# Kernel optimization log

Measured on AMD Instinct MI355X. Metric: run time of the kernel, lower is better.

Reference implementation:

```python
import jax, jax.numpy as jnp
import numpy as np
from jax import lax

NB = 8          # num_blocks
THRESH = 0.01   # sparsity_threshold


def _clinear(z, wr, wi, bias):
    # complex linear y = z @ W^T + b with W = wr + i*wi, z complex
    # (c+id)(a+ib) = (ca - db) + i(cb + da)  -- same math as the torch
    # Karatsuba decomposition (k1-k3, k1+k2).
    zr, zi = z.real, z.imag
    yr = jnp.einsum('...i,oi->...o', zr, wr) - jnp.einsum('...i,oi->...o', zi, wi)
    yi = jnp.einsum('...i,oi->...o', zr, wi) + jnp.einsum('...i,oi->...o', zi, wr)
    y = lax.complex(yr, yi)
    return y + lax.complex(bias[:, 0], bias[:, 1])


def _softshrink(v, t):
    return jnp.where(v > t, v - t, jnp.where(v < -t, v + t, jnp.zeros_like(v)))


def setup_inputs() -> dict:
    key = jax.random.key(0)
    ks = jax.random.split(key, 7)
    B, H, W, D = 4, 128, 128, 768
    bs = D // NB          # block_size = 96
    hid = bs              # hidden_size_factor = 1.0
    scale = np.sqrt(0.5).astype(np.float32)
    kaiming = 1.0 / np.sqrt(bs)
    x = jax.random.normal(ks[0], (B, H, W, D), dtype=jnp.float32)
    # ComplexLinear weights: nn.Linear init then scaled by sqrt(0.5)
    w1r = jax.random.uniform(ks[1], (hid, bs), jnp.float32, -kaiming, kaiming) * scale
    w1i = jax.random.uniform(ks[2], (hid, bs), jnp.float32, -kaiming, kaiming) * scale
    b1 = jax.random.normal(ks[3], (hid, 2), dtype=jnp.float32) * 0.02
    kaiming2 = 1.0 / np.sqrt(hid)
    w2r = jax.random.uniform(ks[4], (bs, hid), jnp.float32, -kaiming2, kaiming2) * scale
    w2i = jax.random.uniform(ks[5], (bs, hid), jnp.float32, -kaiming2, kaiming2) * scale
    b2 = jax.random.normal(ks[6], (bs, 2), dtype=jnp.float32) * 0.02
    return {"x": x, "w1r": w1r, "w1i": w1i, "b1": b1,
            "w2r": w2r, "w2i": w2i, "b2": b2}


def reference(x, w1r, w1i, b1, w2r, w2i, b2):
    B, H, W, D = x.shape
    bs = D // NB
    bias = x  # direct_skip=True -> identity skip
    # ortho-normalized real FFT over spatial dims (1,2)
    xf = jnp.fft.rfftn(x, s=(H, W), axes=(1, 2), norm='ortho')  # [B,H,Fw,D] c64
    Fw = xf.shape[2]
    xb = xf.reshape(B, H, Fw, NB, bs)
    h = _clinear(xb, w1r, w1i, b1)
    h = lax.complex(jax.nn.relu(h.real), jax.nn.relu(h.imag))  # ComplexReLU
    y = _clinear(h, w2r, w2i, b2)
    y = y.reshape(B, H, Fw, D)
    # componentwise softshrink (by_magnitude=False)
    y = lax.complex(_softshrink(y.real, THRESH), _softshrink(y.imag, THRESH))
    out = jnp.fft.irfftn(y, s=(H, W), axes=(1, 2), norm='ortho')
    return out + bias
```

## Files before the change

### kernel.cpp

```cpp
#include <hip/hip_runtime.h>
#include <hip/hip_bf16.h>
#include <cstdio>

#define TPB 256
#define B_ 4
#define H_ 128
#define W_ 128
#define D_ 768
#define FW 65
#define BH_ 512
#define THRESH_ 0.01f
#define NEG_TWO_PI_OVER_128 (-0.04908738521234052f)

typedef short bf16x8 __attribute__((ext_vector_type(8)));
typedef float f32x4 __attribute__((ext_vector_type(4)));


__device__ __forceinline__ unsigned pk(float lo, float hi) {
  __hip_bfloat162 h2 = __float22bfloat162_rn(make_float2(lo, hi));
  return *(unsigned*)&h2;
}
__device__ __forceinline__ float2 upk(unsigned u) {
  return __bfloat1622float2(*(__hip_bfloat162*)&u);
}
__device__ __forceinline__ int drev(int k) {
  return ((k & 3) << 5) | (((k >> 2) & 3) << 3) | (((k >> 4) & 3) << 1) | ((k >> 6) & 1);
}

template <bool FWD>
__device__ __forceinline__ void bfly4(float* re, float* im, int i0, int i1, int i2, int i3,
                                      float c1, float s1, float c2, float s2, float c3, float s3) {
  const float x0r = re[i0], x0i = im[i0], x1r = re[i1], x1i = im[i1];
  const float x2r = re[i2], x2i = im[i2], x3r = re[i3], x3i = im[i3];
  const float v0r = x0r + x2r, v0i = x0i + x2i, v2r = x0r - x2r, v2i = x0i - x2i;
  const float v1r = x1r + x3r, v1i = x1i + x3i, v3r = x1r - x3r, v3i = x1i - x3i;
  float u1r, u1i, u3r, u3i;
  if (FWD) { u1r = v2r + v3i; u1i = v2i - v3r; u3r = v2r - v3i; u3i = v2i + v3r; }
  else     { u1r = v2r - v3i; u1i = v2i + v3r; u3r = v2r + v3i; u3i = v2i - v3r; }
  const float u2r = v0r - v1r, u2i = v0i - v1i;
  re[i0] = v0r + v1r; im[i0] = v0i + v1i;
  re[i1] = u1r * c1 - u1i * s1; im[i1] = u1r * s1 + u1i * c1;
  re[i2] = u2r * c2 - u2i * s2; im[i2] = u2r * s2 + u2i * c2;
  re[i3] = u3r * c3 - u3i * s3; im[i3] = u3r * s3 + u3i * c3;
}

template <bool FWD>
__device__ __forceinline__ void run_stage(float* re, float* im, int t,
                                          int npmask, int npbits, int span, int twm,
                                          const float* twr, const float* twi) {
#pragma unroll
  for (int it = 0; it < 4; ++it) {
    const int gid = it * TPB + t;
    const int cc = gid & 31, g = gid >> 5;
    const int np = g & npmask, blk = g >> npbits;
    const int base = blk * (span << 2) + np;
    const int i0 = base * 32 + cc, i1 = (base + span) * 32 + cc;
    const int i2 = (base + 2 * span) * 32 + cc, i3 = (base + 3 * span) * 32 + cc;
    const int tb = np * twm;
    float c1 = twr[tb], s1 = twi[tb];
    float c2 = twr[2 * tb], s2 = twi[2 * tb];
    float c3 = twr[3 * tb], s3 = twi[3 * tb];
    if (!FWD) { s1 = -s1; s2 = -s2; s3 = -s3; }
    bfly4<FWD>(re, im, i0, i1, i2, i3, c1, s1, c2, s2, c3, s3);
  }
  __syncthreads();
}

__device__ __forceinline__ void run_stage_dit(float* re, float* im, int t,
                                              int npmask, int npbits, int span, int twm,
                                              const float* twr, const float* twi) {
#pragma unroll
  for (int it = 0; it < 4; ++it) {
    const int gid = it * TPB + t;
    const int cc = gid & 31, g = gid >> 5;
    const int np = g & npmask, blk = g >> npbits;
    const int base = blk * (span << 2) + np;
    const int i0 = base * 32 + cc, i1 = (base + span) * 32 + cc;
    const int i2 = (base + 2 * span) * 32 + cc, i3 = (base + 3 * span) * 32 + cc;
    const int tb = np * twm;
    const float c1 = twr[tb], s1 = twi[tb];
    const float c2 = twr[2 * tb], s2 = twi[2 * tb];
    const float c3 = twr[3 * tb], s3 = twi[3 * tb];
    const float t0r = re[i0], t0i = im[i0];
    const float y1r = re[i1], y1i = im[i1], y2r = re[i2], y2i = im[i2], y3r = re[i3], y3i = im[i3];
    const float t1r = y1r * c1 + y1i * s1, t1i = y1i * c1 - y1r * s1;
    const float t2r = y2r * c2 + y2i * s2, t2i = y2i * c2 - y2r * s2;
    const float t3r = y3r * c3 + y3i * s3, t3i = y3i * c3 - y3r * s3;
    const float w0r = t0r + t2r, w0i = t0i + t2i, w2r = t0r - t2r, w2i = t0i - t2i;
    const float w1r = t1r + t3r, w1i = t1i + t3i, w3r = t1r - t3r, w3i = t1i - t3i;
    re[i0] = w0r + w1r; im[i0] = w0i + w1i;
    re[i1] = w2r - w3i; im[i1] = w2i + w3r;
    re[i2] = w0r - w1r; im[i2] = w0i - w1i;
    re[i3] = w2r + w3i; im[i3] = w2i - w3r;
  }
  __syncthreads();
}

__device__ __forceinline__ void run_r2(float* re, float* im, int t) {
#pragma unroll
  for (int it = 0; it < 8; ++it) {
    const int pid = it * TPB + t;
    const int cc = pid & 31, p = pid >> 5;
    const int i0 = (2 * p) * 32 + cc, i1 = i0 + 32;
    const float ar = re[i0], ai = im[i0], br = re[i1], bi = im[i1];
    re[i0] = ar + br; im[i0] = ai + bi;
    re[i1] = ar - br; im[i1] = ai - bi;
  }
  __syncthreads();
}

#define TW_INIT() do { if (t < 128) { float s_, c_; \
    __sincosf(NEG_TWO_PI_OVER_128 * (float)t, &s_, &c_); twr[t] = c_; twi[t] = s_; } } while (0)

__global__ __launch_bounds__(TPB) void k_wpack(const float* __restrict__ w1r,
                                               const float* __restrict__ w1i,
                                               const float* __restrict__ w2r,
                                               const float* __restrict__ w2i,
                                               unsigned short* __restrict__ wp) {
  const int tid = blockIdx.x * TPB + threadIdx.x;
  if (tid >= 2 * 36864) return;
  const int L = tid / 36864, rem = tid % 36864;
  const int n = rem / 192, k = rem % 192;
  const int c = k >> 1, s = k & 1, o = n >> 1, t = n & 1;
  const float* wr = L ? w2r : w1r;
  const float* wi = L ? w2i : w1i;
  const float val = (s == 0) ? (t == 0 ? wr[o * 96 + c] : wi[o * 96 + c])
                             : (t == 0 ? -wi[o * 96 + c] : wr[o * 96 + c]);
  __hip_bfloat16 h = __float2bfloat16(val);
  const int idx = ((n * 6 + (k >> 5)) * 4 + ((k >> 3) & 3)) * 8 + (k & 7);
  wp[L * 36864 + idx] = *(unsigned short*)&h;
}

__global__ __launch_bounds__(TPB) void k_fwd_w(const float* __restrict__ x,
                                               unsigned* __restrict__ fq) {
  __shared__ float re[4096], im[4096], twr[128], twi[128];
  const int t = threadIdx.x;
  const int bh = blockIdx.x;
  const int d0 = blockIdx.y << 6;
  TW_INIT();
  const float2* xp = (const float2*)(x + (size_t)bh * 98304 + d0);
#pragma unroll
  for (int it = 0; it < 16; ++it) {
    const int w = (it << 3) + (t >> 5), c = t & 31;
    const float2 v = xp[w * 384 + c];
    re[w * 32 + c] = v.x; im[w * 32 + c] = v.y;
  }
  __syncthreads();
  run_stage<true>(re, im, t, 31, 5, 32, 1, twr, twi);
  run_stage<true>(re, im, t, 7, 3, 8, 4, twr, twi);
  run_stage<true>(re, im, t, 1, 1, 2, 16, twr, twi);
  run_r2(re, im, t);
#pragma unroll
  for (int it = 0; it < 9; ++it) {
    const int idx = it * TPB + t;
    if (idx < FW * 32) {
      const int q = idx >> 5, c = idx & 31;
      const int sq = drev(q), sm = drev((128 - q) & 127);
      const float a = re[sq * 32 + c], b = im[sq * 32 + c];
      const float cr = re[sm * 32 + c], dr = -im[sm * 32 + c];
      const float hsc = 0.00390625f;
      const float xer = (a + cr) * hsc, xei = (b + dr) * hsc;
      const float xor_ = (b - dr) * hsc, xoi = (cr - a) * hsc;
      *(uint2*)(fq + (size_t)(bh * FW + q) * 768 + d0 + 2 * c) =
          make_uint2(pk(xer, xei), pk(xor_, xoi));
    }
  }
}

__global__ __launch_bounds__(TPB) void k_fwd_h(unsigned* __restrict__ fq) {
  __shared__ float re[4096], im[4096], twr[128], twi[128];
  const int t = threadIdx.x;
  const int b = blockIdx.x, fw = blockIdx.y, d0 = blockIdx.z << 5;
  TW_INIT();
  unsigned* fp = fq + (size_t)(b * 128 * FW + fw) * 768 + d0;
#pragma unroll
  for (int it = 0; it < 16; ++it) {
    const int h = (it << 3) + (t >> 5), c = t & 31;
    const float2 v = upk(fp[(size_t)h * (FW * 768) + c]);
    re[h * 32 + c] = v.x; im[h * 32 + c] = v.y;
  }
  __syncthreads();
  run_stage<true>(re, im, t, 31, 5, 32, 1, twr, twi);
  run_stage<true>(re, im, t, 7, 3, 8, 4, twr, twi);
  run_stage<true>(re, im, t, 1, 1, 2, 16, twr, twi);
  run_r2(re, im, t);
#pragma unroll
  for (int it = 0; it < 16; ++it) {
    const int h = (it << 3) + (t >> 5), c = t & 31;
    fp[(size_t)h * (FW * 768) + c] = pk(re[h * 32 + c], im[h * 32 + c]);
  }
}

__global__ __launch_bounds__(TPB, 2) void k_mlp_mfma(unsigned* __restrict__ fq,
    const bf16x8* __restrict__ wpb,
    const float* __restrict__ b1, const float* __restrict__ b2) {
  __shared__ __align__(16) char lds[49152];
  const int t  = threadIdx.x;
  const int wv = t >> 6;
  const int l  = t & 63;
  const int c16 = l & 15, g = l >> 4, low3 = l & 7;
  const int n0 = wv * 48;
  const int P0 = blockIdx.x << 7;

  const uint4* src = (const uint4*)(fq + (size_t)P0 * 96);
#pragma unroll
  for (int it = 0; it < 12; ++it) {
    const int q = it * TPB + t;
    const int row = q / 24, f = q % 24;
    *(uint4*)(lds + row * 384 + ((f * 16) ^ ((row & 7) << 4))) = src[q];
  }
  __syncthreads();

  f32x4 acc[8][3];
  float bs0 = b1[n0 + c16], bs1 = b1[n0 + 16 + c16], bs2 = b1[n0 + 32 + c16];

#pragma unroll
  for (int mt = 0; mt < 8; ++mt)
#pragma unroll
    for (int np = 0; np < 3; ++np) acc[mt][np] = (f32x4)0.f;
  for (int kk = 0; kk < 6; ++kk) {
    bf16x8 a[8];
#pragma unroll
    for (int mt = 0; mt < 8; ++mt) {
      const int row = (mt << 4) + c16;
      a[mt] = *(const bf16x8*)(lds + row * 384 + ((kk * 64 + g * 16) ^ (low3 << 4)));
    }
    bf16x8 bfr[3];
#pragma unroll
    for (int np = 0; np < 3; ++np) bfr[np] = wpb[((n0 + np * 16 + c16) * 6 + kk) * 4 + g];
#pragma unroll
    for (int mt = 0; mt < 8; ++mt)
#pragma unroll
      for (int np = 0; np < 3; ++np)
        acc[mt][np] = __builtin_amdgcn_mfma_f32_16x16x32_bf16(a[mt], bfr[np], acc[mt][np], 0, 0, 0);
  }
  __syncthreads();
#pragma unroll
  for (int mt = 0; mt < 8; ++mt)
#pragma unroll
    for (int np = 0; np < 3; ++np) {
      const int col = n0 + np * 16 + c16;
      const float bb = np == 0 ? bs0 : (np == 1 ? bs1 : bs2);
#pragma unroll
      for (int r = 0; r < 4; ++r) {
        const int row = (mt << 4) + (g << 2) + r;
        const float vv = fmaxf(acc[mt][np][r] + bb, 0.f);
        __hip_bfloat16 hb = __float2bfloat16(vv);
        *(unsigned short*)(lds + row * 384 + ((2 * col) ^ ((row & 7) << 4))) = *(unsigned short*)&hb;
      }
    }
  __syncthreads();

  bs0 = b2[n0 + c16]; bs1 = b2[n0 + 16 + c16]; bs2 = b2[n0 + 32 + c16];
#pragma unroll
  for (int mt = 0; mt < 8; ++mt)
#pragma unroll
    for (int np = 0; np < 3; ++np) acc[mt][np] = (f32x4)0.f;
  const bf16x8* wpb2 = wpb + 4608;
  for (int kk = 0; kk < 6; ++kk) {
    bf16x8 a[8];
#pragma unroll
    for (int mt = 0; mt < 8; ++mt) {
      const int row = (mt << 4) + c16;
      a[mt] = *(const bf16x8*)(lds + row * 384 + ((kk * 64 + g * 16) ^ (low3 << 4)));
    }
    bf16x8 bfr[3];
#pragma unroll
    for (int np = 0; np < 3; ++np) bfr[np] = wpb2[((n0 + np * 16 + c16) * 6 + kk) * 4 + g];
#pragma unroll
    for (int mt = 0; mt < 8; ++mt)
#pragma unroll
      for (int np = 0; np < 3; ++np)
        acc[mt][np] = __builtin_amdgcn_mfma_f32_16x16x32_bf16(a[mt], bfr[np], acc[mt][np], 0, 0, 0);
  }
  unsigned short* fq16 = (unsigned short*)fq;
#pragma unroll
  for (int mt = 0; mt < 8; ++mt)
#pragma unroll
    for (int np = 0; np < 3; ++np) {
      const int col = n0 + np * 16 + c16;
      const float bb = np == 0 ? bs0 : (np == 1 ? bs1 : bs2);
#pragma unroll
      for (int r = 0; r < 4; ++r) {
        const int row = (mt << 4) + (g << 2) + r;
        float vv = acc[mt][np][r] + bb;
        vv = (vv > THRESH_) ? (vv - THRESH_) : ((vv < -THRESH_) ? (vv + THRESH_) : 0.f);
        __hip_bfloat16 hb = __float2bfloat16(vv);
        fq16[(size_t)(P0 + row) * 192 + col] = *(unsigned short*)&hb;
      }
    }
}

__global__ __launch_bounds__(TPB) void k_inv_h(unsigned* __restrict__ fq) {
  __shared__ float re[4096], im[4096], twr[128], twi[128];
  const int t = threadIdx.x;
  const int b = blockIdx.x, fw = blockIdx.y, d0 = blockIdx.z << 5;
  TW_INIT();
  unsigned* fp = fq + (size_t)(b * 128 * FW + fw) * 768 + d0;
#pragma unroll
  for (int it = 0; it < 16; ++it) {
    const int h = (it << 3) + (t >> 5), c = t & 31;
    const float2 v = upk(fp[(size_t)h * (FW * 768) + c]);
    re[h * 32 + c] = v.x; im[h * 32 + c] = v.y;
  }
  __syncthreads();
  run_r2(re, im, t);
  run_stage_dit(re, im, t, 1, 1, 2, 16, twr, twi);
  run_stage_dit(re, im, t, 7, 3, 8, 4, twr, twi);
  run_stage_dit(re, im, t, 31, 5, 32, 1, twr, twi);
#pragma unroll
  for (int it = 0; it < 16; ++it) {
    const int h = (it << 3) + (t >> 5), c = t & 31;
    fp[(size_t)h * (FW * 768) + c] = pk(re[h * 32 + c], im[h * 32 + c]);
  }
}

__global__ __launch_bounds__(TPB) void k_inv_w(const unsigned* __restrict__ fq,
                                               const float* __restrict__ x,
                                               float* __restrict__ out) {
  __shared__ float re[4096], im[4096], twr[128], twi[128];
  const int t = threadIdx.x;
  const int bh = blockIdx.x;
  const int d0 = blockIdx.y << 6;
  TW_INIT();
#pragma unroll
  for (int it = 0; it < 9; ++it) {
    const int idx = it * TPB + t;
    if (idx < FW * 32) {
      const int q = idx >> 5, c = idx & 31;
      const uint2 vv = *(const uint2*)(fq + (size_t)(bh * FW + q) * 768 + d0 + 2 * c);
      const float2 e = upk(vv.x), o = upk(vv.y);
      re[q * 32 + c] = e.x - o.y; im[q * 32 + c] = e.y + o.x;
      if (q >= 1 && q <= 63) {
        re[(128 - q) * 32 + c] = e.x + o.y;
        im[(128 - q) * 32 + c] = o.x - e.y;
      }
    }
  }
  __syncthreads();
  run_stage<false>(re, im, t, 31, 5, 32, 1, twr, twi);
  run_stage<false>(re, im, t, 7, 3, 8, 4, twr, twi);
  run_stage<false>(re, im, t, 1, 1, 2, 16, twr, twi);
  run_r2(re, im, t);
  const float sc = 0.0078125f;
#pragma unroll
  for (int it = 0; it < 16; ++it) {
    const int w = (it << 3) + (t >> 5), c = t & 31;
    const int s = drev(w);
    const float yr = re[s * 32 + c] * sc, yi = im[s * 32 + c] * sc;
    const size_t fi = (size_t)bh * 49152 + w * 384 + (d0 >> 1) + c;
    const float2 xv = ((const float2*)x)[fi];
    ((float2*)out)[fi] = make_float2(yr + xv.x, yi + xv.y);
  }
}

extern "C" void kernel_launch(void* const* d_in, const int* in_sizes, int n_in,
                              void* d_out, int out_size, void* d_ws, size_t ws_size,
                              hipStream_t stream) {
  const float* x   = (const float*)d_in[0];
  const float* w1r = (const float*)d_in[1];
  const float* w1i = (const float*)d_in[2];
  const float* b1  = (const float*)d_in[3];
  const float* w2r = (const float*)d_in[4];
  const float* w2i = (const float*)d_in[5];
  const float* b2  = (const float*)d_in[6];
  unsigned* fq = (unsigned*)d_ws;
  float* out = (float*)d_out;

  const size_t need = (size_t)BH_ * FW * 768 * 4;
  if (ws_size < need) {
    fprintf(stderr, "kernel_launch: ws too small (%zu < %zu)\n", ws_size, need);
    return;
  }

  unsigned short* wp = (unsigned short*)d_out;

  k_wpack<<<dim3(288), TPB, 0, stream>>>(w1r, w1i, w2r, w2i, wp);
  k_fwd_w<<<dim3(BH_, 12), TPB, 0, stream>>>(x, fq);
  k_fwd_h<<<dim3(B_, FW, 24), TPB, 0, stream>>>(fq);
  k_mlp_mfma<<<dim3(2080), TPB, 0, stream>>>(fq, (const bf16x8*)wp, b1, b2);
  k_inv_h<<<dim3(B_, FW, 24), TPB, 0, stream>>>(fq);
  k_inv_w<<<dim3(BH_, 12), TPB, 0, stream>>>(fq, x, out);
}
```

Measured before the change: 354.7 us.

## Fuse H-axis FFT, complex MLP and inverse H-axis FFT into one kernel

Merges the forward column FFT, both complex-linear MFMA layers and the inverse column FFT into a single 512-thread kernel. Each block holds one 128x96 channel block for one (b, fw) in LDS as fp32 with a swizzled layout. The MLP reads its operands directly from the FFT result and writes the hidden activations back to LDS. This removes two global round trips of the bf16 spectrum and two kernel launches. In exchange, each block uses about 99KB of LDS, which allows only one block per CU. The grid also shrinks to 2080 blocks of 512 threads, which may reduce latency hiding.

```diff
diff --git a/kernel.cpp b/kernel.cpp
--- a/kernel.cpp
+++ b/kernel.cpp
@@ -66,17 +66,63 @@
   __syncthreads();
 }
 
-__device__ __forceinline__ void run_stage_dit(float* re, float* im, int t,
-                                              int npmask, int npbits, int span, int twm,
-                                              const float* twr, const float* twi) {
-#pragma unroll
-  for (int it = 0; it < 4; ++it) {
-    const int gid = it * TPB + t;
-    const int cc = gid & 31, g = gid >> 5;
+__device__ __forceinline__ void run_r2(float* re, float* im, int t) {
+#pragma unroll
+  for (int it = 0; it < 8; ++it) {
+    const int pid = it * TPB + t;
+    const int cc = pid & 31, p = pid >> 5;
+    const int i0 = (2 * p) * 32 + cc, i1 = i0 + 32;
+    const float ar = re[i0], ai = im[i0], br = re[i1], bi = im[i1];
+    re[i0] = ar + br; im[i0] = ai + bi;
+    re[i1] = ar - br; im[i1] = ai - bi;
+  }
+  __syncthreads();
+}
+
+#define TW_INIT() do { if (t < 128) { float s_, c_; \
+    __sincosf(NEG_TWO_PI_OVER_128 * (float)t, &s_, &c_); twr[t] = c_; twi[t] = s_; } } while (0)
+
+__device__ __forceinline__ int midx(int s, int c) { return s * 96 + (c ^ ((s & 7) << 2)); }
+
+template <bool FWD>
+__device__ __forceinline__ void stage512(float* re, float* im, int t,
+                                         int npmask, int npbits, int span, int twm,
+                                         const float* twr, const float* twi) {
+#pragma unroll
+  for (int it = 0; it < 6; ++it) {
+    const int gid = it * 512 + t;
+    const int c5 = gid & 31;
+    const int rest = gid >> 5;
+    const int g = rest & 31, cblk = rest >> 5;
+    const int col = cblk * 32 + c5;
     const int np = g & npmask, blk = g >> npbits;
     const int base = blk * (span << 2) + np;
-    const int i0 = base * 32 + cc, i1 = (base + span) * 32 + cc;
-    const int i2 = (base + 2 * span) * 32 + cc, i3 = (base + 3 * span) * 32 + cc;
+    const int i0 = midx(base, col), i1 = midx(base + span, col);
+    const int i2 = midx(base + 2 * span, col), i3 = midx(base + 3 * span, col);
+    const int tb = np * twm;
+    float c1 = twr[tb], s1 = twi[tb];
+    float c2 = twr[2 * tb], s2 = twi[2 * tb];
+    float c3 = twr[3 * tb], s3 = twi[3 * tb];
+    if (!FWD) { s1 = -s1; s2 = -s2; s3 = -s3; }
+    bfly4<FWD>(re, im, i0, i1, i2, i3, c1, s1, c2, s2, c3, s3);
+  }
+  __syncthreads();
+}
+
+__device__ __forceinline__ void dit512(float* re, float* im, int t,
+                                       int npmask, int npbits, int span, int twm,
+                                       const float* twr, const float* twi) {
+#pragma unroll
+  for (int it = 0; it < 6; ++it) {
+    const int gid = it * 512 + t;
+    const int c5 = gid & 31;
+    const int rest = gid >> 5;
+    const int g = rest & 31, cblk = rest >> 5;
+    const int col = cblk * 32 + c5;
+    const int np = g & npmask, blk = g >> npbits;
+    const int base = blk * (span << 2) + np;
+    const int i0 = midx(base, col), i1 = midx(base + span, col);
+    const int i2 = midx(base + 2 * span, col), i3 = midx(base + 3 * span, col);
     const int tb = np * twm;
     const float c1 = twr[tb], s1 = twi[tb];
     const float c2 = twr[2 * tb], s2 = twi[2 * tb];
@@ -96,21 +142,21 @@
   __syncthreads();
 }
 
-__device__ __forceinline__ void run_r2(float* re, float* im, int t) {
-#pragma unroll
-  for (int it = 0; it < 8; ++it) {
-    const int pid = it * TPB + t;
-    const int cc = pid & 31, p = pid >> 5;
-    const int i0 = (2 * p) * 32 + cc, i1 = i0 + 32;
+__device__ __forceinline__ void r2_512(float* re, float* im, int t) {
+#pragma unroll
+  for (int it = 0; it < 12; ++it) {
+    const int gid = it * 512 + t;
+    const int c5 = gid & 31;
+    const int rest = gid >> 5;
+    const int p = rest & 63, cblk = rest >> 6;
+    const int col = cblk * 32 + c5;
+    const int i0 = midx(2 * p, col), i1 = midx(2 * p + 1, col);
     const float ar = re[i0], ai = im[i0], br = re[i1], bi = im[i1];
     re[i0] = ar + br; im[i0] = ai + bi;
     re[i1] = ar - br; im[i1] = ai - bi;
   }
   __syncthreads();
 }
-
-#define TW_INIT() do { if (t < 128) { float s_, c_; \
-    __sincosf(NEG_TWO_PI_OVER_128 * (float)t, &s_, &c_); twr[t] = c_; twi[t] = s_; } } while (0)
 
 __global__ __launch_bounds__(TPB) void k_wpack(const float* __restrict__ w1r,
                                                const float* __restrict__ w1i,
@@ -167,151 +213,154 @@
   }
 }
 
-__global__ __launch_bounds__(TPB) void k_fwd_h(unsigned* __restrict__ fq) {
-  __shared__ float re[4096], im[4096], twr[128], twi[128];
-  const int t = threadIdx.x;
-  const int b = blockIdx.x, fw = blockIdx.y, d0 = blockIdx.z << 5;
-  TW_INIT();
-  unsigned* fp = fq + (size_t)(b * 128 * FW + fw) * 768 + d0;
-#pragma unroll
-  for (int it = 0; it < 16; ++it) {
-    const int h = (it << 3) + (t >> 5), c = t & 31;
-    const float2 v = upk(fp[(size_t)h * (FW * 768) + c]);
-    re[h * 32 + c] = v.x; im[h * 32 + c] = v.y;
-  }
-  __syncthreads();
-  run_stage<true>(re, im, t, 31, 5, 32, 1, twr, twi);
-  run_stage<true>(re, im, t, 7, 3, 8, 4, twr, twi);
-  run_stage<true>(re, im, t, 1, 1, 2, 16, twr, twi);
-  run_r2(re, im, t);
-#pragma unroll
-  for (int it = 0; it < 16; ++it) {
-    const int h = (it << 3) + (t >> 5), c = t & 31;
-    fp[(size_t)h * (FW * 768) + c] = pk(re[h * 32 + c], im[h * 32 + c]);
-  }
-}
-
-__global__ __launch_bounds__(TPB, 2) void k_mlp_mfma(unsigned* __restrict__ fq,
+__global__ __launch_bounds__(512, 1) void k_mid(unsigned* __restrict__ fq,
     const bf16x8* __restrict__ wpb,
     const float* __restrict__ b1, const float* __restrict__ b2) {
-  __shared__ __align__(16) char lds[49152];
-  const int t  = threadIdx.x;
-  const int wv = t >> 6;
-  const int l  = t & 63;
-  const int c16 = l & 15, g = l >> 4, low3 = l & 7;
-  const int n0 = wv * 48;
-  const int P0 = blockIdx.x << 7;
-
-  const uint4* src = (const uint4*)(fq + (size_t)P0 * 96);
+  extern __shared__ float sm[];
+  float* re  = sm;
+  float* im  = sm + 12288;
+  float* twr = sm + 24576;
+  float* twi = sm + 24704;
+  const int t = threadIdx.x;
+  const int blk = blockIdx.x, fw = blockIdx.y, b = blockIdx.z;
+  TW_INIT();
+  unsigned* fp = fq + ((size_t)(b * 128) * FW + fw) * 768 + blk * 96;
+
 #pragma unroll
   for (int it = 0; it < 12; ++it) {
-    const int q = it * TPB + t;
-    const int row = q / 24, f = q % 24;
-    *(uint4*)(lds + row * 384 + ((f * 16) ^ ((row & 7) << 4))) = src[q];
-  }
-  __syncthreads();
-
-  f32x4 acc[8][3];
-  float bs0 = b1[n0 + c16], bs1 = b1[n0 + 16 + c16], bs2 = b1[n0 + 32 + c16];
-
-#pragma unroll
-  for (int mt = 0; mt < 8; ++mt)
+    const int gid = it * 512 + t;
+    const int uc = gid % 48, h = gid / 48;
+    const uint2 v = *(const uint2*)(fp + (size_t)h * (FW * 768) + 2 * uc);
+    const float2 e0 = upk(v.x), e1 = upk(v.y);
+    const int idx = midx(h, 2 * uc);
+    *(float2*)(re + idx) = make_float2(e0.x, e1.x);
+    *(float2*)(im + idx) = make_float2(e0.y, e1.y);
+  }
+  __syncthreads();
+
+  stage512<true>(re, im, t, 31, 5, 32, 1, twr, twi);
+  stage512<true>(re, im, t, 7, 3, 8, 4, twr, twi);
+  stage512<true>(re, im, t, 1, 1, 2, 16, twr, twi);
+  r2_512(re, im, t);
+
+  const int wv = t >> 6, l = t & 63;
+  const int c16 = l & 15, g4 = l >> 4;
+  const int wr = wv >> 2, wc = wv & 3;
+  const int n0 = wc * 48, row0 = wr * 64;
+
+  float bA[3], bB[3];
+#pragma unroll
+  for (int np = 0; np < 3; ++np) {
+    bA[np] = b1[n0 + np * 16 + c16];
+    bB[np] = b2[n0 + np * 16 + c16];
+  }
+
+  f32x4 acc[4][3];
+#pragma unroll
+  for (int mt = 0; mt < 4; ++mt)
 #pragma unroll
     for (int np = 0; np < 3; ++np) acc[mt][np] = (f32x4)0.f;
+
   for (int kk = 0; kk < 6; ++kk) {
-    bf16x8 a[8];
-#pragma unroll
-    for (int mt = 0; mt < 8; ++mt) {
-      const int row = (mt << 4) + c16;
-      a[mt] = *(const bf16x8*)(lds + row * 384 + ((kk * 64 + g * 16) ^ (low3 << 4)));
+    bf16x8 a[4];
+#pragma unroll
+    for (int mt = 0; mt < 4; ++mt) {
+      const int row = row0 + mt * 16 + c16;
+      const int idx = midx(row, kk * 16 + g4 * 4);
+      const f32x4 r4 = *(const f32x4*)(re + idx);
+      const f32x4 i4 = *(const f32x4*)(im + idx);
+      unsigned u[4];
+#pragma unroll
+      for (int j = 0; j < 4; ++j) u[j] = pk(r4[j], i4[j]);
+      a[mt] = *(bf16x8*)u;
     }
     bf16x8 bfr[3];
 #pragma unroll
-    for (int np = 0; np < 3; ++np) bfr[np] = wpb[((n0 + np * 16 + c16) * 6 + kk) * 4 + g];
-#pragma unroll
-    for (int mt = 0; mt < 8; ++mt)
+    for (int np = 0; np < 3; ++np) bfr[np] = wpb[((n0 + np * 16 + c16) * 6 + kk) * 4 + g4];
+#pragma unroll
+    for (int mt = 0; mt < 4; ++mt)
 #pragma unroll
       for (int np = 0; np < 3; ++np)
         acc[mt][np] = __builtin_amdgcn_mfma_f32_16x16x32_bf16(a[mt], bfr[np], acc[mt][np], 0, 0, 0);
   }
   __syncthreads();
-#pragma unroll
-  for (int mt = 0; mt < 8; ++mt)
+
+#pragma unroll
+  for (int mt = 0; mt < 4; ++mt)
 #pragma unroll
     for (int np = 0; np < 3; ++np) {
       const int col = n0 + np * 16 + c16;
-      const float bb = np == 0 ? bs0 : (np == 1 ? bs1 : bs2);
+      const int ch = col >> 1;
+      float* dst = (col & 1) ? im : re;
 #pragma unroll
       for (int r = 0; r < 4; ++r) {
-        const int row = (mt << 4) + (g << 2) + r;
-        const float vv = fmaxf(acc[mt][np][r] + bb, 0.f);
-        __hip_bfloat16 hb = __float2bfloat16(vv);
-        *(unsigned short*)(lds + row * 384 + ((2 * col) ^ ((row & 7) << 4))) = *(unsigned short*)&hb;
+        const int row = row0 + mt * 16 + g4 * 4 + r;
+        dst[midx(row, ch) + (ch ^ ((row & 7) << 2)) - (ch ^ ((row & 7) << 2))] =
+            fmaxf(acc[mt][np][r] + bA[np], 0.f);
       }
     }
   __syncthreads();
 
-  bs0 = b2[n0 + c16]; bs1 = b2[n0 + 16 + c16]; bs2 = b2[n0 + 32 + c16];
-#pragma unroll
-  for (int mt = 0; mt < 8; ++mt)
+#pragma unroll
+  for (int mt = 0; mt < 4; ++mt)
 #pragma unroll
     for (int np = 0; np < 3; ++np) acc[mt][np] = (f32x4)0.f;
   const bf16x8* wpb2 = wpb + 4608;
   for (int kk = 0; kk < 6; ++kk) {
-    bf16x8 a[8];
-#pragma unroll
-    for (int mt = 0; mt < 8; ++mt) {
-      const int row = (mt << 4) + c16;
-      a[mt] = *(const bf16x8*)(lds + row * 384 + ((kk * 64 + g * 16) ^ (low3 << 4)));
+    bf16x8 a[4];
+#pragma unroll
+    for (int mt = 0; mt < 4; ++mt) {
+      const int row = row0 + mt * 16 + c16;
+      const int idx = midx(row, kk * 16 + g4 * 4);
+      const f32x4 r4 = *(const f32x4*)(re + idx);
+      const f32x4 i4 = *(const f32x4*)(im + idx);
+      unsigned u[4];
+#pragma unroll
+      for (int j = 0; j < 4; ++j) u[j] = pk(r4[j], i4[j]);
+      a[mt] = *(bf16x8*)u;
     }
     bf16x8 bfr[3];
 #pragma unroll
-    for (int np = 0; np < 3; ++np) bfr[np] = wpb2[((n0 + np * 16 + c16) * 6 + kk) * 4 + g];
-#pragma unroll
-    for (int mt = 0; mt < 8; ++mt)
+    for (int np = 0; np < 3; ++np) bfr[np] = wpb2[((n0 + np * 16 + c16) * 6 + kk) * 4 + g4];
+#pragma unroll
+    for (int mt = 0; mt < 4; ++mt)
 #pragma unroll
       for (int np = 0; np < 3; ++np)
         acc[mt][np] = __builtin_amdgcn_mfma_f32_16x16x32_bf16(a[mt], bfr[np], acc[mt][np], 0, 0, 0);
   }
-  unsigned short* fq16 = (unsigned short*)fq;
-#pragma unroll
-  for (int mt = 0; mt < 8; ++mt)
+  __syncthreads();
+
+#pragma unroll
+  for (int mt = 0; mt < 4; ++mt)
 #pragma unroll
     for (int np = 0; np < 3; ++np) {
       const int col = n0 + np * 16 + c16;
-      const float bb = np == 0 ? bs0 : (np == 1 ? bs1 : bs2);
+      const int ch = col >> 1;
+      float* dst = (col & 1) ? im : re;
 #pragma unroll
       for (int r = 0; r < 4; ++r) {
-        const int row = (mt << 4) + (g << 2) + r;
-        float vv = acc[mt][np][r] + bb;
+        const int row = row0 + mt * 16 + g4 * 4 + r;
+        float vv = acc[mt][np][r] + bB[np];
         vv = (vv > THRESH_) ? (vv - THRESH_) : ((vv < -THRESH_) ? (vv + THRESH_) : 0.f);
-        __hip_bfloat16 hb = __float2bfloat16(vv);
-        fq16[(size_t)(P0 + row) * 192 + col] = *(unsigned short*)&hb;
+        dst[midx(row, ch)] = vv;
       }
     }
-}
-
-__global__ __launch_bounds__(TPB) void k_inv_h(unsigned* __restrict__ fq) {
-  __shared__ float re[4096], im[4096], twr[128], twi[128];
-  const int t = threadIdx.x;
-  const int b = blockIdx.x, fw = blockIdx.y, d0 = blockIdx.z << 5;
-  TW_INIT();
-  unsigned* fp = fq + (size_t)(b * 128 * FW + fw) * 768 + d0;
-#pragma unroll
-  for (int it = 0; it < 16; ++it) {
-    const int h = (it << 3) + (t >> 5), c = t & 31;
-    const float2 v = upk(fp[(size_t)h * (FW * 768) + c]);
-    re[h * 32 + c] = v.x; im[h * 32 + c] = v.y;
-  }
-  __syncthreads();
-  run_r2(re, im, t);
-  run_stage_dit(re, im, t, 1, 1, 2, 16, twr, twi);
-  run_stage_dit(re, im, t, 7, 3, 8, 4, twr, twi);
-  run_stage_dit(re, im, t, 31, 5, 32, 1, twr, twi);
-#pragma unroll
-  for (int it = 0; it < 16; ++it) {
-    const int h = (it << 3) + (t >> 5), c = t & 31;
-    fp[(size_t)h * (FW * 768) + c] = pk(re[h * 32 + c], im[h * 32 + c]);
+  __syncthreads();
+
+  r2_512(re, im, t);
+  dit512(re, im, t, 1, 1, 2, 16, twr, twi);
+  dit512(re, im, t, 7, 3, 8, 4, twr, twi);
+  dit512(re, im, t, 31, 5, 32, 1, twr, twi);
+
+#pragma unroll
+  for (int it = 0; it < 12; ++it) {
+    const int gid = it * 512 + t;
+    const int uc = gid % 48, h = gid / 48;
+    const int idx = midx(h, 2 * uc);
+    const float2 r2v = *(const float2*)(re + idx);
+    const float2 i2v = *(const float2*)(im + idx);
+    *(uint2*)(fp + (size_t)h * (FW * 768) + 2 * uc) =
+        make_uint2(pk(r2v.x, i2v.x), pk(r2v.y, i2v.y));
   }
 }
 
@@ -375,10 +424,11 @@
 
   unsigned short* wp = (unsigned short*)d_out;
 
+  const int MID_SMEM = (24576 + 256) * 4;
+  hipFuncSetAttribute((const void*)k_mid, hipFuncAttributeMaxDynamicSharedMemorySize, MID_SMEM);
+
   k_wpack<<<dim3(288), TPB, 0, stream>>>(w1r, w1i, w2r, w2i, wp);
   k_fwd_w<<<dim3(BH_, 12), TPB, 0, stream>>>(x, fq);
-  k_fwd_h<<<dim3(B_, FW, 24), TPB, 0, stream>>>(fq);
-  k_mlp_mfma<<<dim3(2080), TPB, 0, stream>>>(fq, (const bf16x8*)wp, b1, b2);
-  k_inv_h<<<dim3(B_, FW, 24), TPB, 0, stream>>>(fq);
+  k_mid<<<dim3(8, FW, B_), 512, MID_SMEM, stream>>>(fq, (const bf16x8*)wp, b1, b2);
   k_inv_w<<<dim3(BH_, 12), TPB, 0, stream>>>(fq, x, out);
 }
```

New measurement: 503.6 us. 42.0% more time.

## Register-resident H-axis FFT stages and smaller MLP tiles for occupancy

Applied to the files above, without the earlier changes.

The forward and inverse height FFT kernels now keep data in registers for fused radix-4 stages. Only one shared-memory transpose sits between the register passes, replacing four shared-memory round trips each followed by a barrier. The MLP MFMA kernel halves its row tile from 128 to 64 points, halving LDS and accumulators so four blocks per CU fit, and doubles the grid. This cuts LDS traffic and barriers in the FFT, and raises occupancy in the MLP at the cost of more blocks and weight reloads.

```diff
diff --git a/kernel.cpp b/kernel.cpp
--- a/kernel.cpp
+++ b/kernel.cpp
@@ -44,6 +44,35 @@
   re[i3] = u3r * c3 - u3i * s3; im[i3] = u3r * s3 + u3i * c3;
 }
 
+__device__ __forceinline__ void fbf4r(float& x0r, float& x0i, float& x1r, float& x1i,
+                                      float& x2r, float& x2i, float& x3r, float& x3i,
+                                      float c1, float s1, float c2, float s2, float c3, float s3) {
+  const float v0r = x0r + x2r, v0i = x0i + x2i, v2r = x0r - x2r, v2i = x0i - x2i;
+  const float v1r = x1r + x3r, v1i = x1i + x3i, v3r = x1r - x3r, v3i = x1i - x3i;
+  const float u1r = v2r + v3i, u1i = v2i - v3r;
+  const float u3r = v2r - v3i, u3i = v2i + v3r;
+  const float u2r = v0r - v1r, u2i = v0i - v1i;
+  x0r = v0r + v1r;            x0i = v0i + v1i;
+  x1r = u1r * c1 - u1i * s1;  x1i = u1r * s1 + u1i * c1;
+  x2r = u2r * c2 - u2i * s2;  x2i = u2r * s2 + u2i * c2;
+  x3r = u3r * c3 - u3i * s3;  x3i = u3r * s3 + u3i * c3;
+}
+
+__device__ __forceinline__ void ibf4r(float& x0r, float& x0i, float& x1r, float& x1i,
+                                      float& x2r, float& x2i, float& x3r, float& x3i,
+                                      float c1, float s1, float c2, float s2, float c3, float s3) {
+  const float t0r = x0r, t0i = x0i;
+  const float t1r = x1r * c1 + x1i * s1, t1i = x1i * c1 - x1r * s1;
+  const float t2r = x2r * c2 + x2i * s2, t2i = x2i * c2 - x2r * s2;
+  const float t3r = x3r * c3 + x3i * s3, t3i = x3i * c3 - x3r * s3;
+  const float w0r = t0r + t2r, w0i = t0i + t2i, w2r = t0r - t2r, w2i = t0i - t2i;
+  const float w1r = t1r + t3r, w1i = t1i + t3i, w3r = t1r - t3r, w3i = t1i - t3i;
+  x0r = w0r + w1r; x0i = w0i + w1i;
+  x1r = w2r - w3i; x1i = w2i + w3r;
+  x2r = w0r - w1r; x2i = w0i - w1i;
+  x3r = w2r + w3i; x3i = w2i - w3r;
+}
+
 template <bool FWD>
 __device__ __forceinline__ void run_stage(float* re, float* im, int t,
                                           int npmask, int npbits, int span, int twm,
@@ -62,36 +91,6 @@
     float c3 = twr[3 * tb], s3 = twi[3 * tb];
     if (!FWD) { s1 = -s1; s2 = -s2; s3 = -s3; }
     bfly4<FWD>(re, im, i0, i1, i2, i3, c1, s1, c2, s2, c3, s3);
-  }
-  __syncthreads();
-}
-
-__device__ __forceinline__ void run_stage_dit(float* re, float* im, int t,
-                                              int npmask, int npbits, int span, int twm,
-                                              const float* twr, const float* twi) {
-#pragma unroll
-  for (int it = 0; it < 4; ++it) {
-    const int gid = it * TPB + t;
-    const int cc = gid & 31, g = gid >> 5;
-    const int np = g & npmask, blk = g >> npbits;
-    const int base = blk * (span << 2) + np;
-    const int i0 = base * 32 + cc, i1 = (base + span) * 32 + cc;
-    const int i2 = (base + 2 * span) * 32 + cc, i3 = (base + 3 * span) * 32 + cc;
-    const int tb = np * twm;
-    const float c1 = twr[tb], s1 = twi[tb];
-    const float c2 = twr[2 * tb], s2 = twi[2 * tb];
-    const float c3 = twr[3 * tb], s3 = twi[3 * tb];
-    const float t0r = re[i0], t0i = im[i0];
-    const float y1r = re[i1], y1i = im[i1], y2r = re[i2], y2i = im[i2], y3r = re[i3], y3i = im[i3];
-    const float t1r = y1r * c1 + y1i * s1, t1i = y1i * c1 - y1r * s1;
-    const float t2r = y2r * c2 + y2i * s2, t2i = y2i * c2 - y2r * s2;
-    const float t3r = y3r * c3 + y3i * s3, t3i = y3i * c3 - y3r * s3;
-    const float w0r = t0r + t2r, w0i = t0i + t2i, w2r = t0r - t2r, w2i = t0i - t2i;
-    const float w1r = t1r + t3r, w1i = t1i + t3i, w3r = t1r - t3r, w3i = t1i - t3i;
-    re[i0] = w0r + w1r; im[i0] = w0i + w1i;
-    re[i1] = w2r - w3i; im[i1] = w2i + w3r;
-    re[i2] = w0r - w1r; im[i2] = w0i - w1i;
-    re[i3] = w2r + w3i; im[i3] = w2i - w3r;
   }
   __syncthreads();
 }
@@ -173,55 +172,90 @@
   const int b = blockIdx.x, fw = blockIdx.y, d0 = blockIdx.z << 5;
   TW_INIT();
   unsigned* fp = fq + (size_t)(b * 128 * FW + fw) * 768 + d0;
-#pragma unroll
-  for (int it = 0; it < 16; ++it) {
-    const int h = (it << 3) + (t >> 5), c = t & 31;
-    const float2 v = upk(fp[(size_t)h * (FW * 768) + c]);
-    re[h * 32 + c] = v.x; im[h * 32 + c] = v.y;
-  }
-  __syncthreads();
-  run_stage<true>(re, im, t, 31, 5, 32, 1, twr, twi);
-  run_stage<true>(re, im, t, 7, 3, 8, 4, twr, twi);
-  run_stage<true>(re, im, t, 1, 1, 2, 16, twr, twi);
-  run_r2(re, im, t);
-#pragma unroll
-  for (int it = 0; it < 16; ++it) {
-    const int h = (it << 3) + (t >> 5), c = t & 31;
-    fp[(size_t)h * (FW * 768) + c] = pk(re[h * 32 + c], im[h * 32 + c]);
-  }
-}
-
-__global__ __launch_bounds__(TPB, 2) void k_mlp_mfma(unsigned* __restrict__ fq,
+  const int c = t & 31, p = t >> 5;
+  const size_t hs = (size_t)FW * 768;
+
+  float vr[4][4], vi[4][4];
+#pragma unroll
+  for (int q = 0; q < 4; ++q)
+#pragma unroll
+    for (int m = 0; m < 4; ++m) {
+      const float2 v = upk(fp[(size_t)(p + 8 * m + 32 * q) * hs + c]);
+      vr[q][m] = v.x; vi[q][m] = v.y;
+    }
+  __syncthreads();
+#pragma unroll
+  for (int m = 0; m < 4; ++m) {
+    const int np = p + 8 * m;
+    fbf4r(vr[0][m], vi[0][m], vr[1][m], vi[1][m], vr[2][m], vi[2][m], vr[3][m], vi[3][m],
+          twr[np], twi[np], twr[2 * np], twi[2 * np], twr[3 * np], twi[3 * np]);
+  }
+#pragma unroll
+  for (int q = 0; q < 4; ++q)
+    fbf4r(vr[q][0], vi[q][0], vr[q][1], vi[q][1], vr[q][2], vi[q][2], vr[q][3], vi[q][3],
+          twr[4 * p], twi[4 * p], twr[8 * p], twi[8 * p], twr[12 * p], twi[12 * p]);
+#pragma unroll
+  for (int q = 0; q < 4; ++q)
+#pragma unroll
+    for (int m = 0; m < 4; ++m) {
+      const int pos = p + 8 * m + 32 * q;
+      re[pos * 32 + c] = vr[q][m]; im[pos * 32 + c] = vi[q][m];
+    }
+  __syncthreads();
+
+#pragma unroll
+  for (int half = 0; half < 2; ++half) {
+    const int g = 8 * half + p;
+    float wr8[8], wi8[8];
+#pragma unroll
+    for (int j = 0; j < 8; ++j) { wr8[j] = re[(8 * g + j) * 32 + c]; wi8[j] = im[(8 * g + j) * 32 + c]; }
+    fbf4r(wr8[0], wi8[0], wr8[2], wi8[2], wr8[4], wi8[4], wr8[6], wi8[6],
+          1.f, 0.f, 1.f, 0.f, 1.f, 0.f);
+    fbf4r(wr8[1], wi8[1], wr8[3], wi8[3], wr8[5], wi8[5], wr8[7], wi8[7],
+          twr[16], twi[16], twr[32], twi[32], twr[48], twi[48]);
+#pragma unroll
+    for (int j = 0; j < 8; j += 2) {
+      const float ar = wr8[j], ai = wi8[j], br = wr8[j + 1], bi = wi8[j + 1];
+      wr8[j] = ar + br; wi8[j] = ai + bi;
+      wr8[j + 1] = ar - br; wi8[j + 1] = ai - bi;
+    }
+#pragma unroll
+    for (int j = 0; j < 8; ++j)
+      fp[(size_t)(8 * g + j) * hs + c] = pk(wr8[j], wi8[j]);
+  }
+}
+
+__global__ __launch_bounds__(TPB, 4) void k_mlp_mfma(unsigned* __restrict__ fq,
     const bf16x8* __restrict__ wpb,
     const float* __restrict__ b1, const float* __restrict__ b2) {
-  __shared__ __align__(16) char lds[49152];
+  __shared__ __align__(16) char lds[24576];
   const int t  = threadIdx.x;
   const int wv = t >> 6;
   const int l  = t & 63;
   const int c16 = l & 15, g = l >> 4, low3 = l & 7;
   const int n0 = wv * 48;
-  const int P0 = blockIdx.x << 7;
+  const int P0 = blockIdx.x << 6;
 
   const uint4* src = (const uint4*)(fq + (size_t)P0 * 96);
 #pragma unroll
-  for (int it = 0; it < 12; ++it) {
+  for (int it = 0; it < 6; ++it) {
     const int q = it * TPB + t;
     const int row = q / 24, f = q % 24;
     *(uint4*)(lds + row * 384 + ((f * 16) ^ ((row & 7) << 4))) = src[q];
   }
   __syncthreads();
 
-  f32x4 acc[8][3];
+  f32x4 acc[4][3];
   float bs0 = b1[n0 + c16], bs1 = b1[n0 + 16 + c16], bs2 = b1[n0 + 32 + c16];
 
 #pragma unroll
-  for (int mt = 0; mt < 8; ++mt)
+  for (int mt = 0; mt < 4; ++mt)
 #pragma unroll
     for (int np = 0; np < 3; ++np) acc[mt][np] = (f32x4)0.f;
   for (int kk = 0; kk < 6; ++kk) {
-    bf16x8 a[8];
-#pragma unroll
-    for (int mt = 0; mt < 8; ++mt) {
+    bf16x8 a[4];
+#pragma unroll
+    for (int mt = 0; mt < 4; ++mt) {
       const int row = (mt << 4) + c16;
       a[mt] = *(const bf16x8*)(lds + row * 384 + ((kk * 64 + g * 16) ^ (low3 << 4)));
     }
@@ -229,14 +263,14 @@
 #pragma unroll
     for (int np = 0; np < 3; ++np) bfr[np] = wpb[((n0 + np * 16 + c16) * 6 + kk) * 4 + g];
 #pragma unroll
-    for (int mt = 0; mt < 8; ++mt)
+    for (int mt = 0; mt < 4; ++mt)
 #pragma unroll
       for (int np = 0; np < 3; ++np)
         acc[mt][np] = __builtin_amdgcn_mfma_f32_16x16x32_bf16(a[mt], bfr[np], acc[mt][np], 0, 0, 0);
   }
   __syncthreads();
 #pragma unroll
-  for (int mt = 0; mt < 8; ++mt)
+  for (int mt = 0; mt < 4; ++mt)
 #pragma unroll
     for (int np = 0; np < 3; ++np) {
       const int col = n0 + np * 16 + c16;
@@ -253,14 +287,14 @@
 
   bs0 = b2[n0 + c16]; bs1 = b2[n0 + 16 + c16]; bs2 = b2[n0 + 32 + c16];
 #pragma unroll
-  for (int mt = 0; mt < 8; ++mt)
+  for (int mt = 0; mt < 4; ++mt)
 #pragma unroll
     for (int np = 0; np < 3; ++np) acc[mt][np] = (f32x4)0.f;
   const bf16x8* wpb2 = wpb + 4608;
   for (int kk = 0; kk < 6; ++kk) {
-    bf16x8 a[8];
-#pragma unroll
-    for (int mt = 0; mt < 8; ++mt) {
+    bf16x8 a[4];
+#pragma unroll
+    for (int mt = 0; mt < 4; ++mt) {
       const int row = (mt << 4) + c16;
       a[mt] = *(const bf16x8*)(lds + row * 384 + ((kk * 64 + g * 16) ^ (low3 << 4)));
     }
@@ -268,14 +302,14 @@
 #pragma unroll
     for (int np = 0; np < 3; ++np) bfr[np] = wpb2[((n0 + np * 16 + c16) * 6 + kk) * 4 + g];
 #pragma unroll
-    for (int mt = 0; mt < 8; ++mt)
+    for (int mt = 0; mt < 4; ++mt)
 #pragma unroll
       for (int np = 0; np < 3; ++np)
         acc[mt][np] = __builtin_amdgcn_mfma_f32_16x16x32_bf16(a[mt], bfr[np], acc[mt][np], 0, 0, 0);
   }
   unsigned short* fq16 = (unsigned short*)fq;
 #pragma unroll
-  for (int mt = 0; mt < 8; ++mt)
+  for (int mt = 0; mt < 4; ++mt)
 #pragma unroll
     for (int np = 0; np < 3; ++np) {
       const int col = n0 + np * 16 + c16;
@@ -297,22 +331,59 @@
   const int b = blockIdx.x, fw = blockIdx.y, d0 = blockIdx.z << 5;
   TW_INIT();
   unsigned* fp = fq + (size_t)(b * 128 * FW + fw) * 768 + d0;
-#pragma unroll
-  for (int it = 0; it < 16; ++it) {
-    const int h = (it << 3) + (t >> 5), c = t & 31;
-    const float2 v = upk(fp[(size_t)h * (FW * 768) + c]);
-    re[h * 32 + c] = v.x; im[h * 32 + c] = v.y;
-  }
-  __syncthreads();
-  run_r2(re, im, t);
-  run_stage_dit(re, im, t, 1, 1, 2, 16, twr, twi);
-  run_stage_dit(re, im, t, 7, 3, 8, 4, twr, twi);
-  run_stage_dit(re, im, t, 31, 5, 32, 1, twr, twi);
-#pragma unroll
-  for (int it = 0; it < 16; ++it) {
-    const int h = (it << 3) + (t >> 5), c = t & 31;
-    fp[(size_t)h * (FW * 768) + c] = pk(re[h * 32 + c], im[h * 32 + c]);
-  }
+  const int c = t & 31, p = t >> 5;
+  const size_t hs = (size_t)FW * 768;
+
+#pragma unroll
+  for (int half = 0; half < 2; ++half) {
+    const int g = 8 * half + p;
+    float wr8[8], wi8[8];
+#pragma unroll
+    for (int j = 0; j < 8; ++j) {
+      const float2 v = upk(fp[(size_t)(8 * g + j) * hs + c]);
+      wr8[j] = v.x; wi8[j] = v.y;
+    }
+    if (half == 0) __syncthreads();
+#pragma unroll
+    for (int j = 0; j < 8; j += 2) {
+      const float ar = wr8[j], ai = wi8[j], br = wr8[j + 1], bi = wi8[j + 1];
+      wr8[j] = ar + br; wi8[j] = ai + bi;
+      wr8[j + 1] = ar - br; wi8[j + 1] = ai - bi;
+    }
+    ibf4r(wr8[0], wi8[0], wr8[2], wi8[2], wr8[4], wi8[4], wr8[6], wi8[6],
+          1.f, 0.f, 1.f, 0.f, 1.f, 0.f);
+    ibf4r(wr8[1], wi8[1], wr8[3], wi8[3], wr8[5], wi8[5], wr8[7], wi8[7],
+          twr[16], twi[16], twr[32], twi[32], twr[48], twi[48]);
+#pragma unroll
+    for (int j = 0; j < 8; ++j) {
+      re[(8 * g + j) * 32 + c] = wr8[j]; im[(8 * g + j) * 32 + c] = wi8[j];
+    }
+  }
+  __syncthreads();
+
+  float vr[4][4], vi[4][4];
+#pragma unroll
+  for (int q = 0; q < 4; ++q)
+#pragma unroll
+    for (int m = 0; m < 4; ++m) {
+      const int pos = p + 8 * m + 32 * q;
+      vr[q][m] = re[pos * 32 + c]; vi[q][m] = im[pos * 32 + c];
+    }
+#pragma unroll
+  for (int q = 0; q < 4; ++q)
+    ibf4r(vr[q][0], vi[q][0], vr[q][1], vi[q][1], vr[q][2], vi[q][2], vr[q][3], vi[q][3],
+          twr[4 * p], twi[4 * p], twr[8 * p], twi[8 * p], twr[12 * p], twi[12 * p]);
+#pragma unroll
+  for (int m = 0; m < 4; ++m) {
+    const int np = p + 8 * m;
+    ibf4r(vr[0][m], vi[0][m], vr[1][m], vi[1][m], vr[2][m], vi[2][m], vr[3][m], vi[3][m],
+          twr[np], twi[np], twr[2 * np], twi[2 * np], twr[3 * np], twi[3 * np]);
+  }
+#pragma unroll
+  for (int q = 0; q < 4; ++q)
+#pragma unroll
+    for (int m = 0; m < 4; ++m)
+      fp[(size_t)(p + 8 * m + 32 * q) * hs + c] = pk(vr[q][m], vi[q][m]);
 }
 
 __global__ __launch_bounds__(TPB) void k_inv_w(const unsigned* __restrict__ fq,
@@ -378,7 +449,7 @@
   k_wpack<<<dim3(288), TPB, 0, stream>>>(w1r, w1i, w2r, w2i, wp);
   k_fwd_w<<<dim3(BH_, 12), TPB, 0, stream>>>(x, fq);
   k_fwd_h<<<dim3(B_, FW, 24), TPB, 0, stream>>>(fq);
-  k_mlp_mfma<<<dim3(2080), TPB, 0, stream>>>(fq, (const bf16x8*)wp, b1, b2);
+  k_mlp_mfma<<<dim3(4160), TPB, 0, stream>>>(fq, (const bf16x8*)wp, b1, b2);
   k_inv_h<<<dim3(B_, FW, 24), TPB, 0, stream>>>(fq);
   k_inv_w<<<dim3(BH_, 12), TPB, 0, stream>>>(fq, x, out);
 }
```

New measurement: 333.3 us. 1.06x faster.
